# Optimization experiments

Measured on AMD Instinct MI355X. Metric: run time of the kernel, lower is better.

Reference implementation:

```python
import jax, jax.numpy as jnp
import numpy as np

BS, C, D_IN, D_OUT, H = 64, 512, 256, 256, 4
HD = D_OUT // H


def setup_inputs() -> dict:
    key = jax.random.key(0)
    ks = jax.random.split(key, 8)
    def xavier(k, shape):
        fan_in, fan_out = shape[-1], shape[-2] if len(shape) > 1 else shape[-1]
        lim = float(np.sqrt(6.0 / (fan_in + fan_out)))
        return jax.random.uniform(k, shape, jnp.float32, -lim, lim)
    return {
        "h": jax.random.normal(ks[0], (BS, C, D_IN), jnp.float32),
        "A_fc": jax.random.uniform(ks[1], (BS, C, C), jnp.float32),
        "W": xavier(ks[2], (D_OUT, D_IN)),            # Linear(in_dim,out_dim,bias=False).weight
        "a": xavier(ks[3], (H, 2 * HD)),               # attention vector per head
        "W1": xavier(ks[4], (64, D_OUT)),              # channel_agg Linear(out_dim,64)
        "b1": jnp.zeros((64,), jnp.float32),
        "W2": xavier(ks[5], (1, 64)),                  # channel_agg Linear(64,1)
        "b2": jnp.zeros((1,), jnp.float32),
    }


def reference(h, A_fc, W, a, W1, b1, W2, b2):
    bs, c, _ = h.shape
    heads, hd = a.shape[0], a.shape[1] // 2
    # Wh: [BS, C, H, hd]
    Wh = (h @ W.T).reshape(bs, c, heads, hd)
    # a . cat(Wh_i, Wh_j) decomposes into two small projections broadcast-added
    e_i = jnp.einsum('nchd,hd->nch', Wh, a[:, :hd])   # varies over node i
    e_j = jnp.einsum('nchd,hd->nch', Wh, a[:, hd:])   # varies over node j
    e = e_i[:, :, None, :] + e_j[:, None, :, :]        # [BS, Ci, Cj, H]
    e = jax.nn.leaky_relu(e, negative_slope=0.2)
    e = jnp.transpose(e, (0, 3, 1, 2))                 # [BS, H, C, C]
    # prior-weighted scores, softmax over neighbors j (dropout = identity in eval)
    attn = jax.nn.softmax(e * A_fc[:, None, :, :], axis=-1)
    # aggregate: [BS,H,C,C] @ [BS,H,C,hd] -> [BS,C,H,hd] -> [BS,C,out_dim]
    h_prime = jnp.einsum('nhij,njhd->nihd', attn, Wh).reshape(bs, c, heads * hd)
    # channel gating MLP + softmax over channel dim
    s = jnp.tanh(h_prime @ W1.T + b1) @ W2.T + b2      # [BS, C, 1]
    w = jax.nn.softmax(s, axis=1)
    return jnp.sum(h_prime * w, axis=1)                # [BS, out_dim]
```

## Files before the change

### kernel.cpp

```cpp
#include <hip/hip_runtime.h>
#include <hip/hip_bf16.h>

#define BS 64
#define C 512
#define DIN 256
#define DOUT 256
#define H 4
#define HD 64

typedef __attribute__((ext_vector_type(8))) short short8;
typedef __attribute__((ext_vector_type(4))) short short4v;
typedef __attribute__((ext_vector_type(4))) float f32x4;

__device__ __forceinline__ short bfc(float f) {
    union { __hip_bfloat16 h; unsigned short s; } u;
    u.h = __float2bfloat16(f);
    return (short)u.s;
}

__device__ __forceinline__ float bf2f(short v) {
    union { unsigned u; float f; } x;
    x.u = ((unsigned)(unsigned short)v) << 16;
    return x.f;
}

__device__ __forceinline__ short8 pack8n(const float* p) {
    short8 r;
#pragma unroll
    for (int i = 0; i < 8; ++i) r[i] = bfc(p[i]);
    return r;
}

__global__ __launch_bounds__(256) void k0_prep(
    const float* __restrict__ W, const float* __restrict__ W1,
    short* __restrict__ Wbf, short* __restrict__ W1bf)
{
    const int idx = blockIdx.x * 256 + threadIdx.x;
    const int l = idx & 63;
    const int lr = l & 15;
    const int g = l >> 4;
    if (idx < 8192) {
        const int unit = idx >> 6;
        const int head = unit >> 5;
        const int ct = (unit >> 3) & 3;
        const int ks = unit & 7;
        const float* p = W + (size_t)(head * 64 + ct * 16 + lr) * DIN + ks * 32 + g * 8;
        float t[8];
        *(float4*)(t)     = *(const float4*)(p);
        *(float4*)(t + 4) = *(const float4*)(p + 4);
        *(short8*)(Wbf + idx * 8) = pack8n(t);
    } else if (idx < 10240) {
        const int j = idx - 8192;
        const int unit = j >> 6;
        const int ct = unit >> 3;
        const int ks = unit & 7;
        const float* p = W1 + (size_t)(ct * 16 + lr) * DOUT + ks * 32 + g * 8;
        float t[8];
        *(float4*)(t)     = *(const float4*)(p);
        *(float4*)(t + 4) = *(const float4*)(p + 4);
        *(short8*)(W1bf + j * 8) = pack8n(t);
    }
}

__global__ __launch_bounds__(256) void k1_gemm(
    const float* __restrict__ hsrc, const short* __restrict__ Wbf,
    const float* __restrict__ avec,
    short* __restrict__ whT, float* __restrict__ ei, float* __restrict__ ej)
{
    __shared__ __align__(16) short hs[64 * 256];
    const int tid = threadIdx.x;
    const int l = tid & 63;
    const int w = tid >> 6;
    const int lr = l & 15;
    const int g = l >> 4;
    const int kg = g * 8;
    const int mtile = blockIdx.x;
    const int row0 = mtile * 64;
    const float L2E = 1.44269504088896f;

#pragma unroll
    for (int it = 0; it < 8; ++it) {
        const int idx = tid + it * 256;
        const int row = idx >> 5;
        const int colg = idx & 31;
        const float* p = hsrc + (size_t)(row0 + row) * DIN + colg * 8;
        float t[8];
        *(float4*)(t)     = *(const float4*)(p);
        *(float4*)(t + 4) = *(const float4*)(p + 4);
        const int off = (row * 512 + colg * 16) ^ ((row & 7) << 4);
        *(short8*)((char*)hs + off) = pack8n(t);
    }
    __syncthreads();

    const int head = w;
    f32x4 acc[4][4];
#pragma unroll
    for (int i = 0; i < 4; ++i)
#pragma unroll
        for (int j = 0; j < 4; ++j) acc[i][j] = f32x4{0.f, 0.f, 0.f, 0.f};

    const short* wfb = Wbf + (size_t)head * 4 * 8 * 512 + l * 8;
    for (int k0 = 0; k0 < DIN; k0 += 32) {
        const int ks = k0 >> 5;
        short8 af[4];
#pragma unroll
        for (int rt = 0; rt < 4; ++rt) {
            const int row = rt * 16 + lr;
            const int off = (row * 512 + (k0 + kg) * 2) ^ ((row & 7) << 4);
            af[rt] = *(const short8*)((const char*)hs + off);
        }
        short8 bfr[4];
#pragma unroll
        for (int ct = 0; ct < 4; ++ct)
            bfr[ct] = *(const short8*)(wfb + (ct * 8 + ks) * 512);
#pragma unroll
        for (int rt = 0; rt < 4; ++rt)
#pragma unroll
            for (int ct = 0; ct < 4; ++ct)
                acc[rt][ct] = __builtin_amdgcn_mfma_f32_16x16x32_bf16(
                    af[rt], bfr[ct], acc[rt][ct], 0, 0, 0);
    }

    float avi[4], avj[4];
#pragma unroll
    for (int ct = 0; ct < 4; ++ct) {
        avi[ct] = avec[head * 2 * HD + ct * 16 + lr];
        avj[ct] = avec[head * 2 * HD + HD + ct * 16 + lr];
    }

    const int jt = mtile & 7;
    const int bb = mtile >> 3;
    short* fragb = whT + (size_t)(bb * H + head) * (HD * C);

#pragma unroll
    for (int rt = 0; rt < 4; ++rt) {
        const int lane2 = lr + 16 * ((rt & 1) * 2 + (g >> 1));
        const int t0 = (g & 1) * 4;
        const int half = rt >> 1;
#pragma unroll
        for (int ct = 0; ct < 4; ++ct) {
            short4v sv;
#pragma unroll
            for (int reg = 0; reg < 4; ++reg) sv[reg] = bfc(acc[rt][ct][reg]);
            *(short4v*)(fragb + (jt * 4 + ct) * 1024 + half * 512 + lane2 * 8 + t0) = sv;
        }
#pragma unroll
        for (int reg = 0; reg < 4; ++reg) {
            const int j = row0 + rt * 16 + g * 4 + reg;
            const int b = j >> 9;
            const int c = j & 511;
            float pi = 0.f, pj = 0.f;
#pragma unroll
            for (int ct = 0; ct < 4; ++ct) {
                pi += acc[rt][ct][reg] * avi[ct];
                pj += acc[rt][ct][reg] * avj[ct];
            }
#pragma unroll
            for (int off = 1; off < 16; off <<= 1) {
                pi += __shfl_xor(pi, off);
                pj += __shfl_xor(pj, off);
            }
            if (lr == 0) {
                ei[(b * H + head) * C + c] = pi * L2E;
                ej[(b * H + head) * C + c] = pj * L2E;
            }
        }
    }
}

__global__ __launch_bounds__(256) void k2_attn(
    const float* __restrict__ Afc, const short* __restrict__ whT,
    const float* __restrict__ ei, const float* __restrict__ ej,
    short* __restrict__ hpb)
{
    __shared__ __align__(16) short alds[16 * 520];
    __shared__ __align__(16) float elds[4 * 512];
    const int tid = threadIdx.x;
    const int l = tid & 63;
    const int hh = tid >> 6;
    const int swz = (blockIdx.x & 7) * 256 + (blockIdx.x >> 3);
    const int b = swz >> 5;
    const int i0 = (swz & 31) * 16;
    const int lr = l & 15;
    const int kg = (l >> 4) * 8;

    {
        const float* asrc = Afc + ((size_t)b * C + i0) * C;
#pragma unroll
        for (int k = 0; k < 4; ++k) {
            const int idx = tid + k * 256;
            const int row = idx >> 6;
            const int colg = idx & 63;
            const float* p = asrc + row * 512 + colg * 8;
            float t[8];
            *(float4*)(t)     = *(const float4*)(p);
            *(float4*)(t + 4) = *(const float4*)(p + 4);
            *(short8*)(alds + row * 520 + colg * 8) = pack8n(t);
        }
        const float* ejsrc = ej + (size_t)b * H * C;
#pragma unroll
        for (int k = 0; k < 2; ++k) {
            const int idx = tid + k * 256;
            *(float4*)(elds + idx * 4) = *(const float4*)(ejsrc + idx * 4);
        }
    }
    __syncthreads();

    f32x4 O[4];
#pragma unroll
    for (int dt = 0; dt < 4; ++dt) O[dt] = f32x4{0.f, 0.f, 0.f, 0.f};
    float ls0 = 0.f, ls1 = 0.f, ls2 = 0.f, ls3 = 0.f;

    const float eiv = ei[(b * H + hh) * C + i0 + lr];
    const short* vpw = whT + (size_t)(b * H + hh) * (HD * C) + l * 8;
    const short* arowp = alds + lr * 520;
    const float* ejl = elds + hh * 512;

    for (int jt = 0; jt < 8; ++jt) {
        const int j0 = jt * 64;

        short8 vf[4][2];
#pragma unroll
        for (int dt = 0; dt < 4; ++dt) {
            vf[dt][0] = *(const short8*)(vpw + dt * 1024);
            vf[dt][1] = *(const short8*)(vpw + dt * 1024 + 512);
        }

        float ejv[16];
        *(float4*)(ejv)      = *(const float4*)(ejl + j0 + kg);
        *(float4*)(ejv + 4)  = *(const float4*)(ejl + j0 + kg + 4);
        *(float4*)(ejv + 8)  = *(const float4*)(ejl + j0 + 32 + kg);
        *(float4*)(ejv + 12) = *(const float4*)(ejl + j0 + 32 + kg + 4);

        union { short8 s; unsigned u[4]; } a0, a1;
        a0.s = *(const short8*)(arowp + j0 + kg);
        a1.s = *(const short8*)(arowp + j0 + 32 + kg);
        float av[16];
#pragma unroll
        for (int i = 0; i < 4; ++i) {
            union { unsigned u; float f; } lo, hi;
            lo.u = a0.u[i] << 16;
            hi.u = a0.u[i] & 0xffff0000u;
            av[2 * i]     = lo.f;
            av[2 * i + 1] = hi.f;
            lo.u = a1.u[i] << 16;
            hi.u = a1.u[i] & 0xffff0000u;
            av[8 + 2 * i]     = lo.f;
            av[8 + 2 * i + 1] = hi.f;
        }

#pragma unroll
        for (int t = 0; t < 16; ++t) {
            const float z = eiv + ejv[t];
            const float zl = fmaxf(z, 0.2f * z);
            av[t] = __builtin_amdgcn_exp2f(zl * av[t]);
        }

        union { short8 s; unsigned u[4]; } P0, P1;
#pragma unroll
        for (int i = 0; i < 4; ++i) {
            const unsigned b0 = __float_as_uint(av[2 * i])     & 0xffff0000u;
            const unsigned b1 = __float_as_uint(av[2 * i + 1]) & 0xffff0000u;
            ls0 += __uint_as_float(b0);
            ls1 += __uint_as_float(b1);
            P0.u[i] = (b0 >> 16) | b1;
            const unsigned c0 = __float_as_uint(av[8 + 2 * i])     & 0xffff0000u;
            const unsigned c1 = __float_as_uint(av[8 + 2 * i + 1]) & 0xffff0000u;
            ls2 += __uint_as_float(c0);
            ls3 += __uint_as_float(c1);
            P1.u[i] = (c0 >> 16) | c1;
        }

#pragma unroll
        for (int dt = 0; dt < 4; ++dt) {
            O[dt] = __builtin_amdgcn_mfma_f32_16x16x32_bf16(P0.s, vf[dt][0], O[dt], 0, 0, 0);
            O[dt] = __builtin_amdgcn_mfma_f32_16x16x32_bf16(P1.s, vf[dt][1], O[dt], 0, 0, 0);
        }
        vpw += 4096;
    }

    float lsum = (ls0 + ls1) + (ls2 + ls3);
    lsum += __shfl_xor(lsum, 16);
    lsum += __shfl_xor(lsum, 32);
    const float inv = 1.0f / lsum;
    float fr[4];
#pragma unroll
    for (int reg = 0; reg < 4; ++reg)
        fr[reg] = __shfl(inv, (l >> 4) * 4 + reg);
#pragma unroll
    for (int dt = 0; dt < 4; ++dt)
#pragma unroll
        for (int reg = 0; reg < 4; ++reg) {
            const int c = i0 + (l >> 4) * 4 + reg;
            hpb[((size_t)b * C + c) * DOUT + hh * HD + dt * 16 + lr] =
                bfc(O[dt][reg] * fr[reg]);
        }
}

__global__ __launch_bounds__(256) void k3_gate(
    const short* __restrict__ hpb, const short* __restrict__ W1bf,
    const float* __restrict__ b1, const float* __restrict__ W2,
    const float* __restrict__ b2, float* __restrict__ sgate)
{
    __shared__ __align__(16) short hs[64 * 256];
    const int t = threadIdx.x;
    const int l = t & 63;
    const int w = t >> 6;
    const int b = blockIdx.x >> 3;
    const int c0 = (blockIdx.x & 7) * 64;
    const int lr = l & 15;
    const int kg = (l >> 4) * 8;

    {
        const short* src = hpb + ((size_t)b * C + c0) * DOUT;
#pragma unroll
        for (int it = 0; it < 8; ++it) {
            const int idx = t + it * 256;
            const int row = idx >> 5;
            const int colg = idx & 31;
            const int off = (row * 512 + colg * 16) ^ ((row & 7) << 4);
            *(short8*)((char*)hs + off) = *(const short8*)(src + row * 256 + colg * 8);
        }
    }
    __syncthreads();

    f32x4 acc[4];
#pragma unroll
    for (int ct = 0; ct < 4; ++ct) acc[ct] = f32x4{0.f, 0.f, 0.f, 0.f};

    const int myrow = w * 16 + lr;
    const short* w1b = W1bf + l * 8;
    for (int k0 = 0; k0 < DOUT; k0 += 32) {
        const int ks = k0 >> 5;
        const int off = (myrow * 512 + (k0 + kg) * 2) ^ ((myrow & 7) << 4);
        const short8 af = *(const short8*)((const char*)hs + off);
#pragma unroll
        for (int ct = 0; ct < 4; ++ct) {
            const short8 bfr = *(const short8*)(w1b + (ct * 8 + ks) * 512);
            acc[ct] = __builtin_amdgcn_mfma_f32_16x16x32_bf16(af, bfr, acc[ct], 0, 0, 0);
        }
    }

    float b1v[4], w2v[4];
#pragma unroll
    for (int ct = 0; ct < 4; ++ct) {
        b1v[ct] = b1[ct * 16 + lr];
        w2v[ct] = W2[ct * 16 + lr];
    }
    const float b2v = b2[0];
#pragma unroll
    for (int reg = 0; reg < 4; ++reg) {
        float val = 0.f;
#pragma unroll
        for (int ct = 0; ct < 4; ++ct)
            val += tanhf(acc[ct][reg] + b1v[ct]) * w2v[ct];
#pragma unroll
        for (int off = 1; off < 16; off <<= 1) val += __shfl_xor(val, off);
        if (lr == 0)
            sgate[b * C + c0 + w * 16 + (l >> 4) * 4 + reg] = val + b2v;
    }
}

__global__ __launch_bounds__(256) void k4a_partial(
    const short* __restrict__ hpb, const float* __restrict__ sgate,
    float* __restrict__ partial)
{
    __shared__ float red[16];
    __shared__ float wlds[64];
    const int t = threadIdx.x;
    const int b = blockIdx.x >> 3;
    const int c0 = (blockIdx.x & 7) * 64;
    const int l = t & 63, w = t >> 6;
    const float L2E = 1.44269504088896f;

    const float s0 = sgate[b * C + t], s1 = sgate[b * C + 256 + t];
    float mx = fmaxf(s0, s1);
#pragma unroll
    for (int off = 1; off < 64; off <<= 1) mx = fmaxf(mx, __shfl_xor(mx, off));
    if (l == 0) red[w] = mx;
    __syncthreads();
    mx = fmaxf(fmaxf(red[0], red[1]), fmaxf(red[2], red[3]));
    float sum = __builtin_amdgcn_exp2f((s0 - mx) * L2E) + __builtin_amdgcn_exp2f((s1 - mx) * L2E);
#pragma unroll
    for (int off = 1; off < 64; off <<= 1) sum += __shfl_xor(sum, off);
    if (l == 0) red[8 + w] = sum;
    __syncthreads();
    sum = red[8] + red[9] + red[10] + red[11];
    const float inv = 1.f / sum;
    if (t < 64)
        wlds[t] = __builtin_amdgcn_exp2f((sgate[b * C + c0 + t] - mx) * L2E) * inv;
    __syncthreads();

    float acc = 0.f;
    const short* base = hpb + ((size_t)b * C + c0) * DOUT + t;
#pragma unroll 4
    for (int c = 0; c < 64; ++c) acc += wlds[c] * bf2f(base[(size_t)c * DOUT]);
    partial[(size_t)blockIdx.x * DOUT + t] = acc;
}

__global__ __launch_bounds__(256) void k4b_reduce(
    const float* __restrict__ partial, float* __restrict__ out)
{
    const int t = threadIdx.x;
    const int b = blockIdx.x;
    float s = 0.f;
#pragma unroll
    for (int k = 0; k < 8; ++k)
        s += partial[(size_t)(b * 8 + k) * DOUT + t];
    out[b * DOUT + t] = s;
}

extern "C" void kernel_launch(void* const* d_in, const int* in_sizes, int n_in,
                              void* d_out, int out_size, void* d_ws, size_t ws_size,
                              hipStream_t stream) {
    const float* hsrc = (const float*)d_in[0];
    const float* Afc  = (const float*)d_in[1];
    const float* W    = (const float*)d_in[2];
    const float* avec = (const float*)d_in[3];
    const float* W1   = (const float*)d_in[4];
    const float* b1   = (const float*)d_in[5];
    const float* W2   = (const float*)d_in[6];
    const float* b2   = (const float*)d_in[7];

    char* ws = (char*)d_ws;
    short* whT   = (short*)(ws);
    float* ei    = (float*)(ws + 16777216);
    float* ej    = (float*)(ws + 17301504);
    short* hpb   = (short*)(ws + 17825792);
    float* sg    = (float*)(ws + 34603008);
    float* parts = (float*)(ws + 34734080);
    short* Wbf   = (short*)(ws + 35258368);
    short* W1bf  = (short*)(ws + 35389440);

    hipLaunchKernelGGL(k0_prep, dim3(40), dim3(256), 0, stream, W, W1, Wbf, W1bf);
    hipLaunchKernelGGL(k1_gemm, dim3(512), dim3(256), 0, stream, hsrc, Wbf, avec, whT, ei, ej);
    hipLaunchKernelGGL(k2_attn, dim3(2048), dim3(256), 0, stream, Afc, whT, ei, ej, hpb);
    hipLaunchKernelGGL(k3_gate, dim3(512), dim3(256), 0, stream, hpb, W1bf, b1, W2, b2, sg);
    hipLaunchKernelGGL(k4a_partial, dim3(512), dim3(256), 0, stream, hpb, sg, parts);
    hipLaunchKernelGGL(k4b_reduce, dim3(64), dim3(256), 0, stream, parts, (float*)d_out);
}
```

Baseline: 68.99 us.

## Fuse channel gating MLP into attention kernel epilogue

The gating MLP (h_prime @ W1^T, tanh, dot with W2) now runs inside the attention kernel's epilogue. The bf16 h_prime tile is staged in LDS, each wave computes 16 of the 64 hidden units with MFMA, and the partial sums are combined across waves through shared memory. This removes the separate gate kernel launch and its re-read of h_prime from global memory. In exchange the attention kernel gets extra syncthreads, LDS traffic and register pressure.

After: 67.15 us. 2.7% less time.

```diff
diff --git a/kernel.cpp b/kernel.cpp
--- a/kernel.cpp
+++ b/kernel.cpp
@@ -171,10 +171,13 @@
 __global__ __launch_bounds__(256) void k2_attn(
     const float* __restrict__ Afc, const short* __restrict__ whT,
     const float* __restrict__ ei, const float* __restrict__ ej,
-    short* __restrict__ hpb)
+    const short* __restrict__ W1bf, const float* __restrict__ b1,
+    const float* __restrict__ W2, const float* __restrict__ b2,
+    short* __restrict__ hpb, float* __restrict__ sgate)
 {
     __shared__ __align__(16) short alds[16 * 520];
     __shared__ __align__(16) float elds[4 * 512];
+    __shared__ float ps[4][16];
     const int tid = threadIdx.x;
     const int l = tid & 63;
     const int hh = tid >> 6;
@@ -287,78 +290,40 @@
 #pragma unroll
     for (int reg = 0; reg < 4; ++reg)
         fr[reg] = __shfl(inv, (l >> 4) * 4 + reg);
+
+    __syncthreads();
+    short* gt = alds;
 #pragma unroll
     for (int dt = 0; dt < 4; ++dt)
 #pragma unroll
         for (int reg = 0; reg < 4; ++reg) {
-            const int c = i0 + (l >> 4) * 4 + reg;
-            hpb[((size_t)b * C + c) * DOUT + hh * HD + dt * 16 + lr] =
-                bfc(O[dt][reg] * fr[reg]);
-        }
-}
-
-__global__ __launch_bounds__(256) void k3_gate(
-    const short* __restrict__ hpb, const short* __restrict__ W1bf,
-    const float* __restrict__ b1, const float* __restrict__ W2,
-    const float* __restrict__ b2, float* __restrict__ sgate)
-{
-    __shared__ __align__(16) short hs[64 * 256];
-    const int t = threadIdx.x;
-    const int l = t & 63;
-    const int w = t >> 6;
-    const int b = blockIdx.x >> 3;
-    const int c0 = (blockIdx.x & 7) * 64;
-    const int lr = l & 15;
-    const int kg = (l >> 4) * 8;
-
-    {
-        const short* src = hpb + ((size_t)b * C + c0) * DOUT;
-#pragma unroll
-        for (int it = 0; it < 8; ++it) {
-            const int idx = t + it * 256;
-            const int row = idx >> 5;
-            const int colg = idx & 31;
-            const int off = (row * 512 + colg * 16) ^ ((row & 7) << 4);
-            *(short8*)((char*)hs + off) = *(const short8*)(src + row * 256 + colg * 8);
-        }
-    }
-    __syncthreads();
-
-    f32x4 acc[4];
-#pragma unroll
-    for (int ct = 0; ct < 4; ++ct) acc[ct] = f32x4{0.f, 0.f, 0.f, 0.f};
-
-    const int myrow = w * 16 + lr;
-    const short* w1b = W1bf + l * 8;
-    for (int k0 = 0; k0 < DOUT; k0 += 32) {
-        const int ks = k0 >> 5;
-        const int off = (myrow * 512 + (k0 + kg) * 2) ^ ((myrow & 7) << 4);
-        const short8 af = *(const short8*)((const char*)hs + off);
-#pragma unroll
-        for (int ct = 0; ct < 4; ++ct) {
-            const short8 bfr = *(const short8*)(w1b + (ct * 8 + ks) * 512);
-            acc[ct] = __builtin_amdgcn_mfma_f32_16x16x32_bf16(af, bfr, acc[ct], 0, 0, 0);
-        }
-    }
-
-    float b1v[4], w2v[4];
-#pragma unroll
-    for (int ct = 0; ct < 4; ++ct) {
-        b1v[ct] = b1[ct * 16 + lr];
-        w2v[ct] = W2[ct * 16 + lr];
-    }
-    const float b2v = b2[0];
+            const int cl = (l >> 4) * 4 + reg;
+            const short v = bfc(O[dt][reg] * fr[reg]);
+            hpb[((size_t)b * C + i0 + cl) * DOUT + hh * HD + dt * 16 + lr] = v;
+            gt[cl * 264 + hh * 64 + dt * 16 + lr] = v;
+        }
+    __syncthreads();
+
+    f32x4 gacc = f32x4{0.f, 0.f, 0.f, 0.f};
+    const short* w1b = W1bf + (hh * 8) * 512 + l * 8;
+#pragma unroll
+    for (int ks = 0; ks < 8; ++ks) {
+        const short8 ga8 = *(const short8*)(gt + lr * 264 + ks * 32 + kg);
+        const short8 gb8 = *(const short8*)(w1b + ks * 512);
+        gacc = __builtin_amdgcn_mfma_f32_16x16x32_bf16(ga8, gb8, gacc, 0, 0, 0);
+    }
+    const float b1v = b1[hh * 16 + lr];
+    const float w2v = W2[hh * 16 + lr];
 #pragma unroll
     for (int reg = 0; reg < 4; ++reg) {
-        float val = 0.f;
-#pragma unroll
-        for (int ct = 0; ct < 4; ++ct)
-            val += tanhf(acc[ct][reg] + b1v[ct]) * w2v[ct];
-#pragma unroll
-        for (int off = 1; off < 16; off <<= 1) val += __shfl_xor(val, off);
-        if (lr == 0)
-            sgate[b * C + c0 + w * 16 + (l >> 4) * 4 + reg] = val + b2v;
-    }
+        float tv = tanhf(gacc[reg] + b1v) * w2v;
+#pragma unroll
+        for (int off = 1; off < 16; off <<= 1) tv += __shfl_xor(tv, off);
+        if (lr == 0) ps[hh][(l >> 4) * 4 + reg] = tv;
+    }
+    __syncthreads();
+    if (tid < 16)
+        sgate[b * C + i0 + tid] = (ps[0][tid] + ps[1][tid]) + (ps[2][tid] + ps[3][tid]) + b2[0];
 }
 
 __global__ __launch_bounds__(256) void k4a_partial(
@@ -434,8 +399,8 @@
 
     hipLaunchKernelGGL(k0_prep, dim3(40), dim3(256), 0, stream, W, W1, Wbf, W1bf);
     hipLaunchKernelGGL(k1_gemm, dim3(512), dim3(256), 0, stream, hsrc, Wbf, avec, whT, ei, ej);
-    hipLaunchKernelGGL(k2_attn, dim3(2048), dim3(256), 0, stream, Afc, whT, ei, ej, hpb);
-    hipLaunchKernelGGL(k3_gate, dim3(512), dim3(256), 0, stream, hpb, W1bf, b1, W2, b2, sg);
+    hipLaunchKernelGGL(k2_attn, dim3(2048), dim3(256), 0, stream,
+                       Afc, whT, ei, ej, W1bf, b1, W2, b2, hpb, sg);
     hipLaunchKernelGGL(k4a_partial, dim3(512), dim3(256), 0, stream, hpb, sg, parts);
     hipLaunchKernelGGL(k4b_reduce, dim3(64), dim3(256), 0, stream, parts, (float*)d_out);
 }
```
